# Performance work log

Hardware: AMD Instinct MI355X
Metric: run time of the kernel (lower is better)

The kernel has to match this reference:

```python
import jax, jax.numpy as jnp
import numpy as np

B, H, Wd = 32, 64, 64
C_IN = 65            # ambient Lorentz dim (1 time + 64 space)
KH = KW = 3          # kernel
OUT = 256            # out_channels (ambient); linear space dim = 255
HCAT = (C_IN - 1) * KH * KW + 1  # 577
CURV = 1.0


def setup_inputs() -> dict:
    key = jax.random.key(0)
    k1, k2, k3 = jax.random.split(key, 3)
    # spatial (tangent-like) components, projected onto the hyperboloid
    v = jax.random.normal(k1, (B, H, Wd, C_IN - 1), dtype=jnp.float32) * 0.5
    t = jnp.sqrt(1.0 / CURV + jnp.sum(v * v, axis=-1, keepdims=True))
    x = jnp.concatenate([t, v], axis=-1)  # valid Lorentz points, (B,H,W,65)
    W = jax.random.normal(k2, (OUT - 1, HCAT), dtype=jnp.float32) * (1.0 / np.sqrt(HCAT))
    b = jnp.zeros((OUT - 1,), dtype=jnp.float32)
    return {"x": x, "W": W, "b": b}


def reference(x, W, b):
    c = CURV
    Bn, Hn, Wn, C = x.shape
    # 'SAME' padding with stride 1, kernel 3 -> pad 1 on each side, edge mode
    xp = jnp.pad(x, ((0, 0), (1, 1), (1, 1), (0, 0)), mode="edge")
    # im2col: stack the KH*KW shifted views -> (B, H, W, N, C)
    slabs = [xp[:, i:i + Hn, j:j + Wn, :] for i in range(KH) for j in range(KW)]
    patches = jnp.stack(slabs, axis=3)
    N = KH * KW
    # Lorentz direct concatenation (HCat):
    # time = sqrt(sum_i t_i^2 - (N-1)/c), space = concat of spatial parts
    t_cat = jnp.sqrt(jnp.sum(patches[..., 0] ** 2, axis=-1) - (N - 1) / c)
    sp = patches[..., 1:].reshape(Bn, Hn, Wn, N * (C - 1))
    h = jnp.concatenate([t_cat[..., None], sp], axis=-1)  # (B,H,W,577)
    # Hyperbolic linear (Lorentz fully-connected): space part is affine map,
    # time part restores the Lorentz constraint <y,y>_L = -1/c
    z = jnp.einsum("bhwi,oi->bhwo", h, W) + b  # (B,H,W,255)
    t_out = jnp.sqrt(1.0 / c + jnp.sum(z * z, axis=-1, keepdims=True))
    return jnp.concatenate([t_out, z], axis=-1)  # (B,H,W,256)
```

## Files before the change

kernel.cpp:

```cpp
#include <hip/hip_runtime.h>
#include <hip/hip_bf16.h>


#define CLAMP63(v) ((v) < 0 ? 0 : ((v) > 63 ? 63 : (v)))

typedef __attribute__((ext_vector_type(8))) short short8;
typedef __attribute__((ext_vector_type(4))) float floatx4;

__device__ __forceinline__ void gl2lds16(const void* g, void* l) {
  __builtin_amdgcn_global_load_lds(
      (const __attribute__((address_space(1))) void*)g,
      (__attribute__((address_space(3))) void*)l, 16, 0, 0);
}

__global__ void prep_x(const float* __restrict__ x, __hip_bfloat16* __restrict__ xs,
                       float* __restrict__ tsq) {
  int idx = blockIdx.x * 256 + threadIdx.x;
  int p = idx >> 3, g = idx & 7;
  const float* src = x + (size_t)p * 65 + 1 + g * 8;
  __align__(16) __hip_bfloat16 tmp[8];
#pragma unroll
  for (int i = 0; i < 8; ++i) tmp[i] = __float2bfloat16(src[i]);
  *(short8*)(xs + (size_t)idx * 8) = *(const short8*)tmp;
  if (g == 0) { float t = x[(size_t)p * 65]; tsq[p] = t * t; }
}

__global__ void prep_w(const float* __restrict__ W, const float* __restrict__ b,
                       __hip_bfloat16* __restrict__ Wb, float* __restrict__ Wt0,
                       float* __restrict__ bp) {
  int n = blockIdx.x;
  for (int k = threadIdx.x; k < 576; k += 256)
    Wb[n * 576 + k] = __float2bfloat16((n < 255) ? W[n * 577 + 1 + k] : 0.f);
  if (threadIdx.x == 0) {
    Wt0[n] = (n < 255) ? W[n * 577] : 0.f;
    bp[n]  = (n < 255) ? b[n] : 0.f;
  }
}

#define STAGE(IT, BUF)                                                          \
  do {                                                                          \
    const int nbr_ = (IT) >> 1;                                                 \
    const int dy_ = nbr_ / 3 - 1, dx_ = nbr_ % 3 - 1;                           \
    const int c0_ = ((IT) & 1) * 32;                                            \
    int y2_ = CLAMP63(a_by + dy_);                                              \
    int x2_ = CLAMP63(a_bx + dx_);                                              \
    gl2lds16(xs + (size_t)((a_bb * 64 + y2_) * 64 + x2_) * 64 + c0_ + a_kg * 8, \
             Ab + (BUF) * 4096 + w * 512);                                      \
    _Pragma("unroll")                                                           \
    for (int j = 0; j < 2; ++j)                                                 \
      gl2lds16(b_src[j] + (IT) * 32, Bb + (BUF) * 8192 + (w * 2 + j) * 512);    \
  } while (0)

__launch_bounds__(512, 4)
__global__ void hypconv_main(const float* __restrict__ tsq,
                             const __hip_bfloat16* __restrict__ xs,
                             const __hip_bfloat16* __restrict__ Wb,
                             const float* __restrict__ Wt0,
                             const float* __restrict__ bp,
                             float* __restrict__ out) {
  __shared__ __align__(16) char smem[49152];
  __shared__ float tc_lds[128];
  ushort* Ab = (ushort*)smem;
  ushort* Bb = (ushort*)(smem + 16384);
  float* zbuf = (float*)smem;

  const int tid = threadIdx.x;
  const int w = tid >> 6, lane = tid & 63;
  const int quad = lane >> 4, ln = lane & 15;
  const int pix_base = blockIdx.x * 128;
  const int m_off = (w >> 2) * 64, n_off = (w & 3) * 64;

  const int a_kg = w >> 1;
  int apix = pix_base + (w & 1) * 64 + lane;
  const int a_bx = apix & 63, a_by = (apix >> 6) & 63, a_bb = apix >> 12;
  const __hip_bfloat16* b_src[2];
#pragma unroll
  for (int j = 0; j < 2; ++j) {
    int c = w * 2 + j;
    b_src[j] = Wb + (size_t)((c & 3) * 64 + lane) * 576 + (c >> 2) * 8;
  }

  floatx4 acc[4][4];
#pragma unroll
  for (int mf = 0; mf < 4; ++mf)
#pragma unroll
    for (int nf = 0; nf < 4; ++nf)
      acc[mf][nf] = (floatx4){0.f, 0.f, 0.f, 0.f};

  STAGE(0, 0);

  if (tid < 128) {
    int pix = pix_base + tid;
    int bx = pix & 63, by = (pix >> 6) & 63, bb = pix >> 12;
    float s = 0.f;
#pragma unroll
    for (int dy = -1; dy <= 1; ++dy) {
      int y2 = CLAMP63(by + dy);
#pragma unroll
      for (int dx = -1; dx <= 1; ++dx) {
        int x2 = CLAMP63(bx + dx);
        s += tsq[(bb * 64 + y2) * 64 + x2];
      }
    }
    tc_lds[tid] = sqrtf(s - 8.0f);
  }

  for (int it = 0; it < 18; ++it) {
    __syncthreads();
    if (it < 17) STAGE(it + 1, (it + 1) & 1);
    const ushort* Ar = Ab + (it & 1) * 4096;
    const ushort* Br = Bb + (it & 1) * 8192;
    short8 af[4], bfr[4];
#pragma unroll
    for (int mf = 0; mf < 4; ++mf)
      af[mf] = *(const short8*)&Ar[(quad * 128 + m_off + mf * 16 + ln) * 8];
#pragma unroll
    for (int nf = 0; nf < 4; ++nf)
      bfr[nf] = *(const short8*)&Br[(quad * 256 + n_off + nf * 16 + ln) * 8];
#pragma unroll
    for (int mf = 0; mf < 4; ++mf)
#pragma unroll
      for (int nf = 0; nf < 4; ++nf)
        acc[mf][nf] = __builtin_amdgcn_mfma_f32_16x16x32_bf16(af[mf], bfr[nf], acc[mf][nf], 0, 0, 0);
  }

  __syncthreads();
  float wn[4], bnv[4];
#pragma unroll
  for (int nf = 0; nf < 4; ++nf) {
    int n = n_off + nf * 16 + ln;
    wn[nf] = Wt0[n];
    bnv[nf] = bp[n];
  }

#pragma unroll
  for (int mf = 0; mf < 4; ++mf) {
#pragma unroll
    for (int r = 0; r < 4; ++r) {
      float tcv = tc_lds[m_off + mf * 16 + quad * 4 + r];
      int lr = (w >> 2) * 16 + quad * 4 + r;
#pragma unroll
      for (int nf = 0; nf < 4; ++nf) {
        float z = acc[mf][nf][r] + bnv[nf] + tcv * wn[nf];
        zbuf[lr * 260 + ((1 + n_off + nf * 16 + ln) & 255)] = z;
      }
    }
    __syncthreads();
#pragma unroll
    for (int rr = 0; rr < 4; ++rr) {
      int lr = w * 4 + rr;
      float4 v = *(const float4*)&zbuf[lr * 260 + lane * 4];
      float ss = v.x * v.x + v.y * v.y + v.z * v.z + v.w * v.w;
      ss += __shfl_xor(ss, 1, 64);
      ss += __shfl_xor(ss, 2, 64);
      ss += __shfl_xor(ss, 4, 64);
      ss += __shfl_xor(ss, 8, 64);
      ss += __shfl_xor(ss, 16, 64);
      ss += __shfl_xor(ss, 32, 64);
      float tout = sqrtf(1.0f + ss);
      if (lane == 0) v.x = tout;
      int m = (lr >> 4) * 64 + mf * 16 + (lr & 15);
      *(float4*)&out[(size_t)(pix_base + m) * 256 + lane * 4] = v;
    }
    if (mf < 3) __syncthreads();
  }
}

extern "C" void kernel_launch(void* const* d_in, const int* in_sizes, int n_in,
                              void* d_out, int out_size, void* d_ws, size_t ws_size,
                              hipStream_t stream) {
  const float* x = (const float*)d_in[0];
  const float* W = (const float*)d_in[1];
  const float* b = (const float*)d_in[2];
  float* out = (float*)d_out;
  char* ws = (char*)d_ws;

  __hip_bfloat16* xs  = (__hip_bfloat16*)(ws);
  __hip_bfloat16* Wb  = (__hip_bfloat16*)(ws + 16777216);
  float*          Wt0 = (float*)(ws + 17072128);
  float*          bp  = (float*)(ws + 17073152);
  float*          tsq = (float*)(ws + 17074176);

  prep_x<<<4096, 256, 0, stream>>>(x, xs, tsq);
  prep_w<<<256,  256, 0, stream>>>(W, b, Wb, Wt0, bp);
  hypconv_main<<<1024, 512, 0, stream>>>(tsq, xs, Wb, Wt0, bp, out);
}
```

Before: 221.5 us.

## Triple-buffer LDS staging with partial vmcnt waits and MFMA priority boost

Replaces the double-buffered K loop with a three-slot LDS ring that prefetches two stages ahead. Each iteration waits only on the oldest outstanding global-to-LDS load (vmcnt(3)) before a raw barrier, so loads overlap more with the MFMA work. The MFMA block is wrapped in s_setprio to favour matrix issue over other waves. The cost is more LDS per block (72 KB instead of 48 KB), which may cut the number of resident blocks per CU and lower latency hiding from occupancy.

Result: slower. 230.0 us (+3.8%).

```diff
diff --git a/kernel.cpp b/kernel.cpp
--- a/kernel.cpp
+++ b/kernel.cpp
@@ -51,6 +51,27 @@
       gl2lds16(b_src[j] + (IT) * 32, Bb + (BUF) * 8192 + (w * 2 + j) * 512);    \
   } while (0)
 
+#define COMPUTE(BC)                                                             \
+  do {                                                                          \
+    const ushort* Ar = Ab + (BC) * 4096;                                        \
+    const ushort* Br = Bb + (BC) * 8192;                                        \
+    short8 af[4], bfr[4];                                                       \
+    _Pragma("unroll")                                                           \
+    for (int mf = 0; mf < 4; ++mf)                                              \
+      af[mf] = *(const short8*)&Ar[(quad * 128 + m_off + mf * 16 + ln) * 8];    \
+    _Pragma("unroll")                                                           \
+    for (int nf = 0; nf < 4; ++nf)                                              \
+      bfr[nf] = *(const short8*)&Br[(quad * 256 + n_off + nf * 16 + ln) * 8];   \
+    __builtin_amdgcn_s_setprio(1);                                              \
+    _Pragma("unroll")                                                           \
+    for (int mf = 0; mf < 4; ++mf)                                              \
+      _Pragma("unroll")                                                         \
+      for (int nf = 0; nf < 4; ++nf)                                            \
+        acc[mf][nf] = __builtin_amdgcn_mfma_f32_16x16x32_bf16(af[mf], bfr[nf],  \
+                                                              acc[mf][nf], 0, 0, 0); \
+    __builtin_amdgcn_s_setprio(0);                                              \
+  } while (0)
+
 __launch_bounds__(512, 4)
 __global__ void hypconv_main(const float* __restrict__ tsq,
                              const __hip_bfloat16* __restrict__ xs,
@@ -58,10 +79,10 @@
                              const float* __restrict__ Wt0,
                              const float* __restrict__ bp,
                              float* __restrict__ out) {
-  __shared__ __align__(16) char smem[49152];
+  __shared__ __align__(16) char smem[73728];
   __shared__ float tc_lds[128];
   ushort* Ab = (ushort*)smem;
-  ushort* Bb = (ushort*)(smem + 16384);
+  ushort* Bb = (ushort*)(smem + 24576);
   float* zbuf = (float*)smem;
 
   const int tid = threadIdx.x;
@@ -86,8 +107,6 @@
 #pragma unroll
     for (int nf = 0; nf < 4; ++nf)
       acc[mf][nf] = (floatx4){0.f, 0.f, 0.f, 0.f};
-
-  STAGE(0, 0);
 
   if (tid < 128) {
     int pix = pix_base + tid;
@@ -105,24 +124,24 @@
     tc_lds[tid] = sqrtf(s - 8.0f);
   }
 
-  for (int it = 0; it < 18; ++it) {
-    __syncthreads();
-    if (it < 17) STAGE(it + 1, (it + 1) & 1);
-    const ushort* Ar = Ab + (it & 1) * 4096;
-    const ushort* Br = Bb + (it & 1) * 8192;
-    short8 af[4], bfr[4];
-#pragma unroll
-    for (int mf = 0; mf < 4; ++mf)
-      af[mf] = *(const short8*)&Ar[(quad * 128 + m_off + mf * 16 + ln) * 8];
-#pragma unroll
-    for (int nf = 0; nf < 4; ++nf)
-      bfr[nf] = *(const short8*)&Br[(quad * 256 + n_off + nf * 16 + ln) * 8];
-#pragma unroll
-    for (int mf = 0; mf < 4; ++mf)
-#pragma unroll
-      for (int nf = 0; nf < 4; ++nf)
-        acc[mf][nf] = __builtin_amdgcn_mfma_f32_16x16x32_bf16(af[mf], bfr[nf], acc[mf][nf], 0, 0, 0);
-  }
+  STAGE(0, 0);
+  STAGE(1, 1);
+
+  int bc = 0;
+  int bs = 2;
+  for (int it = 0; it < 17; ++it) {
+    asm volatile("s_waitcnt vmcnt(3)" ::: "memory");
+    __builtin_amdgcn_s_barrier();
+    __builtin_amdgcn_sched_barrier(0);
+    if (it < 16) STAGE(it + 2, bs);
+    COMPUTE(bc);
+    bc = (bc == 2) ? 0 : bc + 1;
+    bs = (bs == 2) ? 0 : bs + 1;
+  }
+  asm volatile("s_waitcnt vmcnt(0)" ::: "memory");
+  __builtin_amdgcn_s_barrier();
+  __builtin_amdgcn_sched_barrier(0);
+  COMPUTE(2);
 
   __syncthreads();
   float wn[4], bnv[4];
```

## Split output columns across two blocks and finalize time component separately

Applied to the files above, without the earlier changes.

The main GEMM kernel changes from one 512-thread block covering 128 pixels by 256 columns to two 256-thread blocks, each covering 128 columns. A grid swizzle pairs the two column halves of a pixel tile. Each block writes partial sums of squares to a workspace, and a new finalize kernel computes the output time component. The two prep kernels are merged into one launch, and Wb is shifted by one row so column 0 becomes the padding slot. This trades an extra kernel launch and a second read of the A tile per pixel tile for smaller blocks with lower LDS use and more blocks in flight.

Result: slower. 234.0 us (+5.7%).

```diff
diff --git a/kernel.cpp b/kernel.cpp
--- a/kernel.cpp
+++ b/kernel.cpp
@@ -13,52 +13,56 @@
       (__attribute__((address_space(3))) void*)l, 16, 0, 0);
 }
 
-__global__ void prep_x(const float* __restrict__ x, __hip_bfloat16* __restrict__ xs,
-                       float* __restrict__ tsq) {
-  int idx = blockIdx.x * 256 + threadIdx.x;
-  int p = idx >> 3, g = idx & 7;
-  const float* src = x + (size_t)p * 65 + 1 + g * 8;
-  __align__(16) __hip_bfloat16 tmp[8];
+__global__ void prep(const float* __restrict__ x, const float* __restrict__ W,
+                     const float* __restrict__ b,
+                     __hip_bfloat16* __restrict__ xs, float* __restrict__ tsq,
+                     __hip_bfloat16* __restrict__ Wb, float* __restrict__ Wt0,
+                     float* __restrict__ bp) {
+  if (blockIdx.x < 4096) {
+    int idx = blockIdx.x * 256 + threadIdx.x;
+    int p = idx >> 3, g = idx & 7;
+    const float* src = x + (size_t)p * 65 + 1 + g * 8;
+    __align__(16) __hip_bfloat16 tmp[8];
 #pragma unroll
-  for (int i = 0; i < 8; ++i) tmp[i] = __float2bfloat16(src[i]);
-  *(short8*)(xs + (size_t)idx * 8) = *(const short8*)tmp;
-  if (g == 0) { float t = x[(size_t)p * 65]; tsq[p] = t * t; }
-}
-
-__global__ void prep_w(const float* __restrict__ W, const float* __restrict__ b,
-                       __hip_bfloat16* __restrict__ Wb, float* __restrict__ Wt0,
-                       float* __restrict__ bp) {
-  int n = blockIdx.x;
-  for (int k = threadIdx.x; k < 576; k += 256)
-    Wb[n * 576 + k] = __float2bfloat16((n < 255) ? W[n * 577 + 1 + k] : 0.f);
-  if (threadIdx.x == 0) {
-    Wt0[n] = (n < 255) ? W[n * 577] : 0.f;
-    bp[n]  = (n < 255) ? b[n] : 0.f;
+    for (int i = 0; i < 8; ++i) tmp[i] = __float2bfloat16(src[i]);
+    *(short8*)(xs + (size_t)idx * 8) = *(const short8*)tmp;
+    if (g == 0) { float t = x[(size_t)p * 65]; tsq[p] = t * t; }
+  } else {
+    int n = blockIdx.x - 4096;
+    for (int k = threadIdx.x; k < 576; k += 256)
+      Wb[n * 576 + k] = __float2bfloat16((n >= 1) ? W[(n - 1) * 577 + 1 + k] : 0.f);
+    if (threadIdx.x == 0) {
+      Wt0[n] = (n >= 1) ? W[(n - 1) * 577] : 0.f;
+      bp[n]  = (n >= 1) ? b[n - 1] : 0.f;
+    }
   }
 }
 
-#define STAGE(IT, BUF)                                                          \
-  do {                                                                          \
-    const int nbr_ = (IT) >> 1;                                                 \
-    const int dy_ = nbr_ / 3 - 1, dx_ = nbr_ % 3 - 1;                           \
-    const int c0_ = ((IT) & 1) * 32;                                            \
-    int y2_ = CLAMP63(a_by + dy_);                                              \
-    int x2_ = CLAMP63(a_bx + dx_);                                              \
-    gl2lds16(xs + (size_t)((a_bb * 64 + y2_) * 64 + x2_) * 64 + c0_ + a_kg * 8, \
-             Ab + (BUF) * 4096 + w * 512);                                      \
-    _Pragma("unroll")                                                           \
-    for (int j = 0; j < 2; ++j)                                                 \
-      gl2lds16(b_src[j] + (IT) * 32, Bb + (BUF) * 8192 + (w * 2 + j) * 512);    \
+#define STAGE(IT, BUF)                                                            \
+  do {                                                                            \
+    const int nbr_ = (IT) >> 1;                                                   \
+    const int dy_ = nbr_ / 3 - 1, dx_ = nbr_ % 3 - 1;                             \
+    const int c0_ = ((IT) & 1) * 32;                                              \
+    _Pragma("unroll")                                                             \
+    for (int j = 0; j < 2; ++j) {                                                 \
+      int y2_ = CLAMP63(a_by[j] + dy_);                                           \
+      int x2_ = CLAMP63(a_bx[j] + dx_);                                           \
+      gl2lds16(xs + (size_t)((a_bb[j] * 64 + y2_) * 64 + x2_) * 64 + c0_ + w * 8, \
+               Ab + (BUF) * 4096 + w * 1024 + j * 512);                           \
+      gl2lds16(b_src[j] + (IT) * 32,                                              \
+               Bb + (BUF) * 4096 + w * 1024 + j * 512);                           \
+    }                                                                             \
   } while (0)
 
-__launch_bounds__(512, 4)
+__launch_bounds__(256, 4)
 __global__ void hypconv_main(const float* __restrict__ tsq,
                              const __hip_bfloat16* __restrict__ xs,
                              const __hip_bfloat16* __restrict__ Wb,
                              const float* __restrict__ Wt0,
                              const float* __restrict__ bp,
-                             float* __restrict__ out) {
-  __shared__ __align__(16) char smem[49152];
+                             float* __restrict__ out,
+                             float* __restrict__ ssbuf) {
+  __shared__ __align__(16) char smem[32768];
   __shared__ float tc_lds[128];
   ushort* Ab = (ushort*)smem;
   ushort* Bb = (ushort*)(smem + 16384);
@@ -67,18 +71,22 @@
   const int tid = threadIdx.x;
   const int w = tid >> 6, lane = tid & 63;
   const int quad = lane >> 4, ln = lane & 15;
-  const int pix_base = blockIdx.x * 128;
-  const int m_off = (w >> 2) * 64, n_off = (w & 3) * 64;
 
-  const int a_kg = w >> 1;
-  int apix = pix_base + (w & 1) * 64 + lane;
-  const int a_bx = apix & 63, a_by = (apix >> 6) & 63, a_bb = apix >> 12;
+  const int lid = ((blockIdx.x & 7) << 8) + (blockIdx.x >> 3);
+  const int mb = lid >> 1, nb = lid & 1;
+  const int pix_base = mb * 128;
+  const int m_off = (w >> 1) * 64, n_off = (w & 1) * 64;
+
+  int a_bx[2], a_by[2], a_bb[2];
+#pragma unroll
+  for (int j = 0; j < 2; ++j) {
+    int apix = pix_base + j * 64 + lane;
+    a_bx[j] = apix & 63; a_by[j] = (apix >> 6) & 63; a_bb[j] = apix >> 12;
+  }
   const __hip_bfloat16* b_src[2];
 #pragma unroll
-  for (int j = 0; j < 2; ++j) {
-    int c = w * 2 + j;
-    b_src[j] = Wb + (size_t)((c & 3) * 64 + lane) * 576 + (c >> 2) * 8;
-  }
+  for (int j = 0; j < 2; ++j)
+    b_src[j] = Wb + (size_t)(nb * 128 + j * 64 + lane) * 576 + w * 8;
 
   floatx4 acc[4][4];
 #pragma unroll
@@ -86,8 +94,6 @@
 #pragma unroll
     for (int nf = 0; nf < 4; ++nf)
       acc[mf][nf] = (floatx4){0.f, 0.f, 0.f, 0.f};
-
-  STAGE(0, 0);
 
   if (tid < 128) {
     int pix = pix_base + tid;
@@ -105,18 +111,20 @@
     tc_lds[tid] = sqrtf(s - 8.0f);
   }
 
+  STAGE(0, 0);
+
   for (int it = 0; it < 18; ++it) {
     __syncthreads();
     if (it < 17) STAGE(it + 1, (it + 1) & 1);
     const ushort* Ar = Ab + (it & 1) * 4096;
-    const ushort* Br = Bb + (it & 1) * 8192;
+    const ushort* Br = Bb + (it & 1) * 4096;
     short8 af[4], bfr[4];
 #pragma unroll
     for (int mf = 0; mf < 4; ++mf)
       af[mf] = *(const short8*)&Ar[(quad * 128 + m_off + mf * 16 + ln) * 8];
 #pragma unroll
     for (int nf = 0; nf < 4; ++nf)
-      bfr[nf] = *(const short8*)&Br[(quad * 256 + n_off + nf * 16 + ln) * 8];
+      bfr[nf] = *(const short8*)&Br[(quad * 128 + n_off + nf * 16 + ln) * 8];
 #pragma unroll
     for (int mf = 0; mf < 4; ++mf)
 #pragma unroll
@@ -128,7 +136,7 @@
   float wn[4], bnv[4];
 #pragma unroll
   for (int nf = 0; nf < 4; ++nf) {
-    int n = n_off + nf * 16 + ln;
+    int n = nb * 128 + n_off + nf * 16 + ln;
     wn[nf] = Wt0[n];
     bnv[nf] = bp[n];
   }
@@ -138,32 +146,35 @@
 #pragma unroll
     for (int r = 0; r < 4; ++r) {
       float tcv = tc_lds[m_off + mf * 16 + quad * 4 + r];
-      int lr = (w >> 2) * 16 + quad * 4 + r;
+      int lr = (w >> 1) * 16 + quad * 4 + r;
 #pragma unroll
       for (int nf = 0; nf < 4; ++nf) {
         float z = acc[mf][nf][r] + bnv[nf] + tcv * wn[nf];
-        zbuf[lr * 260 + ((1 + n_off + nf * 16 + ln) & 255)] = z;
+        zbuf[lr * 132 + n_off + nf * 16 + ln] = z;
       }
     }
     __syncthreads();
 #pragma unroll
     for (int rr = 0; rr < 4; ++rr) {
-      int lr = w * 4 + rr;
-      float4 v = *(const float4*)&zbuf[lr * 260 + lane * 4];
+      int lr = w * 8 + rr * 2 + (lane >> 5);
+      float4 v = *(const float4*)&zbuf[lr * 132 + (lane & 31) * 4];
       float ss = v.x * v.x + v.y * v.y + v.z * v.z + v.w * v.w;
       ss += __shfl_xor(ss, 1, 64);
       ss += __shfl_xor(ss, 2, 64);
       ss += __shfl_xor(ss, 4, 64);
       ss += __shfl_xor(ss, 8, 64);
       ss += __shfl_xor(ss, 16, 64);
-      ss += __shfl_xor(ss, 32, 64);
-      float tout = sqrtf(1.0f + ss);
-      if (lane == 0) v.x = tout;
       int m = (lr >> 4) * 64 + mf * 16 + (lr & 15);
-      *(float4*)&out[(size_t)(pix_base + m) * 256 + lane * 4] = v;
+      *(float4*)&out[(size_t)(pix_base + m) * 256 + nb * 128 + (lane & 31) * 4] = v;
+      if ((lane & 31) == 0) ssbuf[nb * 131072 + pix_base + m] = ss;
     }
     if (mf < 3) __syncthreads();
   }
+}
+
+__global__ void finalize_t(const float* __restrict__ ssbuf, float* __restrict__ out) {
+  int p = blockIdx.x * 256 + threadIdx.x;
+  out[(size_t)p * 256] = sqrtf(1.0f + ssbuf[p] + ssbuf[131072 + p]);
 }
 
 extern "C" void kernel_launch(void* const* d_in, const int* in_sizes, int n_in,
@@ -180,8 +191,9 @@
   float*          Wt0 = (float*)(ws + 17072128);
   float*          bp  = (float*)(ws + 17073152);
   float*          tsq = (float*)(ws + 17074176);
+  float*          ssb = (float*)(ws + 17598464);
 
-  prep_x<<<4096, 256, 0, stream>>>(x, xs, tsq);
-  prep_w<<<256,  256, 0, stream>>>(W, b, Wb, Wt0, bp);
-  hypconv_main<<<1024, 512, 0, stream>>>(tsq, xs, Wb, Wt0, bp, out);
+  prep<<<4352, 256, 0, stream>>>(x, W, b, xs, tsq, Wb, Wt0, bp);
+  hypconv_main<<<2048, 256, 0, stream>>>(tsq, xs, Wb, Wt0, bp, out, ssb);
+  finalize_t<<<512, 256, 0, stream>>>(ssb, out);
 }
```

## Enlarge GEMM tile to 256x256 with K=64 stages and fuse prep kernels

Applied to the files above, without the earlier changes.

The main kernel now computes 256 pixels by 256 channels per block, up from 128x256. It stages a full 64-channel neighbour slab per iteration, so the loop drops from 18 to 9 iterations with 8x4 MFMA fragments per wave. The two prep kernels are merged into one launch, and the weight layout is shifted so the zero padding channel lands at column 0, which removes the modular index in the epilogue. Blocks are remapped with a swizzled order. The intent is more data reuse per staged byte, fewer barriers and one less launch, at the cost of 128KB of LDS, two-block occupancy and higher register pressure from 128 accumulator floats.

After: 252.8 us. 1.14x slower.

```diff
diff --git a/kernel.cpp b/kernel.cpp
--- a/kernel.cpp
+++ b/kernel.cpp
@@ -13,83 +13,81 @@
       (__attribute__((address_space(3))) void*)l, 16, 0, 0);
 }
 
-__global__ void prep_x(const float* __restrict__ x, __hip_bfloat16* __restrict__ xs,
-                       float* __restrict__ tsq) {
-  int idx = blockIdx.x * 256 + threadIdx.x;
-  int p = idx >> 3, g = idx & 7;
-  const float* src = x + (size_t)p * 65 + 1 + g * 8;
-  __align__(16) __hip_bfloat16 tmp[8];
+__global__ void prep(const float* __restrict__ x, const float* __restrict__ W,
+                     const float* __restrict__ b,
+                     __hip_bfloat16* __restrict__ xs, float* __restrict__ tsq,
+                     __hip_bfloat16* __restrict__ Wb, float* __restrict__ Wt0,
+                     float* __restrict__ bp) {
+  if (blockIdx.x < 4096) {
+    int idx = blockIdx.x * 256 + threadIdx.x;
+    int p = idx >> 3, g = idx & 7;
+    const float* src = x + (size_t)p * 65 + 1 + g * 8;
+    __align__(16) __hip_bfloat16 tmp[8];
 #pragma unroll
-  for (int i = 0; i < 8; ++i) tmp[i] = __float2bfloat16(src[i]);
-  *(short8*)(xs + (size_t)idx * 8) = *(const short8*)tmp;
-  if (g == 0) { float t = x[(size_t)p * 65]; tsq[p] = t * t; }
-}
-
-__global__ void prep_w(const float* __restrict__ W, const float* __restrict__ b,
-                       __hip_bfloat16* __restrict__ Wb, float* __restrict__ Wt0,
-                       float* __restrict__ bp) {
-  int n = blockIdx.x;
-  for (int k = threadIdx.x; k < 576; k += 256)
-    Wb[n * 576 + k] = __float2bfloat16((n < 255) ? W[n * 577 + 1 + k] : 0.f);
-  if (threadIdx.x == 0) {
-    Wt0[n] = (n < 255) ? W[n * 577] : 0.f;
-    bp[n]  = (n < 255) ? b[n] : 0.f;
+    for (int i = 0; i < 8; ++i) tmp[i] = __float2bfloat16(src[i]);
+    *(short8*)(xs + (size_t)idx * 8) = *(const short8*)tmp;
+    if (g == 0) { float t = x[(size_t)p * 65]; tsq[p] = t * t; }
+  } else {
+    int n = blockIdx.x - 4096;
+    for (int k = threadIdx.x; k < 576; k += 256)
+      Wb[n * 576 + k] = __float2bfloat16((n >= 1) ? W[(n - 1) * 577 + 1 + k] : 0.f);
+    if (threadIdx.x == 0) {
+      Wt0[n] = (n >= 1) ? W[(n - 1) * 577] : 0.f;
+      bp[n]  = (n >= 1) ? b[n - 1] : 0.f;
+    }
   }
 }
 
-#define STAGE(IT, BUF)                                                          \
-  do {                                                                          \
-    const int nbr_ = (IT) >> 1;                                                 \
-    const int dy_ = nbr_ / 3 - 1, dx_ = nbr_ % 3 - 1;                           \
-    const int c0_ = ((IT) & 1) * 32;                                            \
-    int y2_ = CLAMP63(a_by + dy_);                                              \
-    int x2_ = CLAMP63(a_bx + dx_);                                              \
-    gl2lds16(xs + (size_t)((a_bb * 64 + y2_) * 64 + x2_) * 64 + c0_ + a_kg * 8, \
-             Ab + (BUF) * 4096 + w * 512);                                      \
-    _Pragma("unroll")                                                           \
-    for (int j = 0; j < 2; ++j)                                                 \
-      gl2lds16(b_src[j] + (IT) * 32, Bb + (BUF) * 8192 + (w * 2 + j) * 512);    \
+#define STAGE(IT, BUF)                                                           \
+  do {                                                                           \
+    const int dy_ = (IT) / 3 - 1, dx_ = (IT) % 3 - 1;                            \
+    int y2_ = CLAMP63(a_by + dy_);                                               \
+    int x2_ = CLAMP63(a_bx + dx_);                                               \
+    const __hip_bfloat16* asrc_ = xs + (size_t)((a_bb * 64 + y2_) * 64 + x2_) * 64; \
+    _Pragma("unroll")                                                            \
+    for (int r_ = 0; r_ < 4; ++r_) {                                             \
+      const int kg_ = 2 * r_ + kg_lo;                                            \
+      gl2lds16(asrc_ + kg_ * 8, Ab + (BUF) * 16384 + r_ * 4096 + w * 512);       \
+      gl2lds16(b_base + (IT) * 64 + kg_ * 8, Bb + (BUF) * 16384 + r_ * 4096 + w * 512); \
+    }                                                                            \
   } while (0)
 
-__launch_bounds__(512, 4)
+__launch_bounds__(512, 2)
 __global__ void hypconv_main(const float* __restrict__ tsq,
                              const __hip_bfloat16* __restrict__ xs,
                              const __hip_bfloat16* __restrict__ Wb,
                              const float* __restrict__ Wt0,
                              const float* __restrict__ bp,
                              float* __restrict__ out) {
-  __shared__ __align__(16) char smem[49152];
-  __shared__ float tc_lds[128];
+  __shared__ __align__(16) char smem[131072];
+  __shared__ float tc_lds[256];
   ushort* Ab = (ushort*)smem;
-  ushort* Bb = (ushort*)(smem + 16384);
+  ushort* Bb = (ushort*)(smem + 65536);
   float* zbuf = (float*)smem;
 
   const int tid = threadIdx.x;
   const int w = tid >> 6, lane = tid & 63;
   const int quad = lane >> 4, ln = lane & 15;
-  const int pix_base = blockIdx.x * 128;
-  const int m_off = (w >> 2) * 64, n_off = (w & 3) * 64;
 
-  const int a_kg = w >> 1;
-  int apix = pix_base + (w & 1) * 64 + lane;
+  const int mb = ((blockIdx.x & 7) << 6) + (blockIdx.x >> 3);
+  const int pix_base = mb * 256;
+  const int wr = w >> 2, wc = w & 3;
+  const int m_off = wr * 128, n_off = wc * 64;
+
+  const int sm = (w & 3) * 64 + lane;
+  const int kg_lo = w >> 2;
+  const int apix = pix_base + sm;
   const int a_bx = apix & 63, a_by = (apix >> 6) & 63, a_bb = apix >> 12;
-  const __hip_bfloat16* b_src[2];
+  const __hip_bfloat16* b_base = Wb + (size_t)sm * 576;
+
+  floatx4 acc[8][4];
 #pragma unroll
-  for (int j = 0; j < 2; ++j) {
-    int c = w * 2 + j;
-    b_src[j] = Wb + (size_t)((c & 3) * 64 + lane) * 576 + (c >> 2) * 8;
-  }
-
-  floatx4 acc[4][4];
-#pragma unroll
-  for (int mf = 0; mf < 4; ++mf)
+  for (int mf = 0; mf < 8; ++mf)
 #pragma unroll
     for (int nf = 0; nf < 4; ++nf)
       acc[mf][nf] = (floatx4){0.f, 0.f, 0.f, 0.f};
 
-  STAGE(0, 0);
-
-  if (tid < 128) {
+  if (tid < 256) {
     int pix = pix_base + tid;
     int bx = pix & 63, by = (pix >> 6) & 63, bb = pix >> 12;
     float s = 0.f;
@@ -105,23 +103,29 @@
     tc_lds[tid] = sqrtf(s - 8.0f);
   }
 
-  for (int it = 0; it < 18; ++it) {
+  STAGE(0, 0);
+
+#pragma unroll
+  for (int it = 0; it < 9; ++it) {
     __syncthreads();
-    if (it < 17) STAGE(it + 1, (it + 1) & 1);
-    const ushort* Ar = Ab + (it & 1) * 4096;
-    const ushort* Br = Bb + (it & 1) * 8192;
-    short8 af[4], bfr[4];
+    if (it < 8) STAGE(it + 1, (it + 1) & 1);
+    const ushort* Ar = Ab + (it & 1) * 16384;
+    const ushort* Br = Bb + (it & 1) * 16384;
 #pragma unroll
-    for (int mf = 0; mf < 4; ++mf)
-      af[mf] = *(const short8*)&Ar[(quad * 128 + m_off + mf * 16 + ln) * 8];
+    for (int ks = 0; ks < 2; ++ks) {
+      short8 af[8], bfr[4];
 #pragma unroll
-    for (int nf = 0; nf < 4; ++nf)
-      bfr[nf] = *(const short8*)&Br[(quad * 256 + n_off + nf * 16 + ln) * 8];
-#pragma unroll
-    for (int mf = 0; mf < 4; ++mf)
+      for (int mf = 0; mf < 8; ++mf)
+        af[mf] = *(const short8*)&Ar[((ks * 4 + quad) * 256 + m_off + mf * 16 + ln) * 8];
 #pragma unroll
       for (int nf = 0; nf < 4; ++nf)
-        acc[mf][nf] = __builtin_amdgcn_mfma_f32_16x16x32_bf16(af[mf], bfr[nf], acc[mf][nf], 0, 0, 0);
+        bfr[nf] = *(const short8*)&Br[((ks * 4 + quad) * 256 + n_off + nf * 16 + ln) * 8];
+#pragma unroll
+      for (int mf = 0; mf < 8; ++mf)
+#pragma unroll
+        for (int nf = 0; nf < 4; ++nf)
+          acc[mf][nf] = __builtin_amdgcn_mfma_f32_16x16x32_bf16(af[mf], bfr[nf], acc[mf][nf], 0, 0, 0);
+    }
   }
 
   __syncthreads();
@@ -134,15 +138,15 @@
   }
 
 #pragma unroll
-  for (int mf = 0; mf < 4; ++mf) {
+  for (int mf = 0; mf < 8; ++mf) {
 #pragma unroll
     for (int r = 0; r < 4; ++r) {
       float tcv = tc_lds[m_off + mf * 16 + quad * 4 + r];
-      int lr = (w >> 2) * 16 + quad * 4 + r;
+      int lr = wr * 16 + quad * 4 + r;
 #pragma unroll
       for (int nf = 0; nf < 4; ++nf) {
         float z = acc[mf][nf][r] + bnv[nf] + tcv * wn[nf];
-        zbuf[lr * 260 + ((1 + n_off + nf * 16 + ln) & 255)] = z;
+        zbuf[lr * 260 + n_off + nf * 16 + ln] = z;
       }
     }
     __syncthreads();
@@ -159,10 +163,10 @@
       ss += __shfl_xor(ss, 32, 64);
       float tout = sqrtf(1.0f + ss);
       if (lane == 0) v.x = tout;
-      int m = (lr >> 4) * 64 + mf * 16 + (lr & 15);
+      int m = (lr >> 4) * 128 + mf * 16 + (lr & 15);
       *(float4*)&out[(size_t)(pix_base + m) * 256 + lane * 4] = v;
     }
-    if (mf < 3) __syncthreads();
+    if (mf < 7) __syncthreads();
   }
 }
 
@@ -181,7 +185,6 @@
   float*          bp  = (float*)(ws + 17073152);
   float*          tsq = (float*)(ws + 17074176);
 
-  prep_x<<<4096, 256, 0, stream>>>(x, xs, tsq);
-  prep_w<<<256,  256, 0, stream>>>(W, b, Wb, Wt0, bp);
-  hypconv_main<<<1024, 512, 0, stream>>>(tsq, xs, Wb, Wt0, bp, out);
+  prep<<<4352, 256, 0, stream>>>(x, W, b, xs, tsq, Wb, Wt0, bp);
+  hypconv_main<<<512, 512, 0, stream>>>(tsq, xs, Wb, Wt0, bp, out);
 }
```
